# Performance work log

Hardware: AMD Instinct MI355X
Metric: run time of the kernel (lower is better)

## Reference

```python
import jax, jax.numpy as jnp
import numpy as np

N_PATCH = 15  # patch_size
M_UNITS = 16  # patches_per_batch


def setup_inputs() -> dict:
    key = jax.random.key(0)
    k1, k2, k3 = jax.random.split(key, 3)
    B, C, H, W = 64, 128, 64, 64
    x = jax.random.normal(k1, (B, C, H, W), dtype=jnp.float32)
    x_cord = jax.random.randint(k2, (B, M_UNITS), 0, W)
    y_cord = jax.random.randint(k3, (B, M_UNITS), 0, H)
    return {"x": x, "x_cord": x_cord, "y_cord": y_cord}


def reference(x, x_cord, y_cord):
    # x: [B, C, H, W]; x_cord/y_cord: [B, M] integer cell indices.
    B, C, H, W = x.shape
    n = N_PATCH
    M = x_cord.shape[1]

    lin = jnp.linspace(-1.0, 1.0, n, dtype=jnp.float32)
    gy, gx = jnp.meshgrid(lin, lin, indexing="ij")  # base_grid: gx = [..,0], gy = [..,1]

    xs = x_cord.reshape(-1).astype(jnp.float32)  # [B*M]
    ys = y_cord.reshape(-1).astype(jnp.float32)
    xs_n = (xs / (W - 1) * 2.0 - 1.0)[:, None, None]
    ys_n = (ys / (H - 1) * 2.0 - 1.0)[:, None, None]
    scale_x = (n - 1) / (W - 1)
    scale_y = (n - 1) / (H - 1)

    # NOTE: the original deliberately adds ys_norm to the x-channel and xs_norm
    # to the y-channel of the grid; we replicate that exactly.
    grid_x_ch = gx * scale_x + ys_n  # grid[..., 0] -> width coord for grid_sample
    grid_y_ch = gy * scale_y + xs_n  # grid[..., 1] -> height coord

    in_bounds = ((grid_x_ch >= -1) & (grid_x_ch <= 1)
                 & (grid_y_ch >= -1) & (grid_y_ch <= 1)).astype(x.dtype)  # [B*M, n, n]

    # grid_sample(mode='nearest', align_corners=True, padding_mode='zeros')
    ix = jnp.round((grid_x_ch + 1.0) * 0.5 * (W - 1)).astype(jnp.int32)
    iy = jnp.round((grid_y_ch + 1.0) * 0.5 * (H - 1)).astype(jnp.int32)
    valid = (ix >= 0) & (ix < W) & (iy >= 0) & (iy < H)
    ixc = jnp.clip(ix, 0, W - 1)
    iyc = jnp.clip(iy, 0, H - 1)

    b_idx = jnp.repeat(jnp.arange(B), M)[:, None, None]  # [B*M,1,1]
    # Direct gather from x (no B*M expanded copy): result [B*M, n, n, C]
    patches = x[b_idx, :, iyc, ixc]
    patches = jnp.transpose(patches, (0, 3, 1, 2))  # [B*M, C, n, n]
    patches = patches * valid[:, None, :, :].astype(x.dtype)  # zero padding

    return jnp.concatenate([patches, in_bounds[:, None, :, :]], axis=1)  # [B*M, C+1, n, n]
```

## Files before the change

### kernel.cpp

```cpp
#include <hip/hip_runtime.h>


constexpr int NP    = 15;
constexpr int NPOS  = NP * NP;
constexpr int CH    = 128;
constexpr int HH    = 64, WW = 64;
constexpr int PLANE = HH * WW;
constexpr int MPB   = 16;
constexpr unsigned PER_PATCH = (CH + 1) * NPOS;

__global__ __launch_bounds__(256)
void patch_swz(const float* __restrict__ x,
               const int* __restrict__ xcord,
               const int* __restrict__ ycord,
               float* __restrict__ out) {
  const int cg = blockIdx.x;
  const int b  = blockIdx.y;
  const int t  = threadIdx.x;

  __shared__ int    sx[MPB], sy[MPB];
  __shared__ float4 s4[HH * (WW / 4)];

  if (t < MPB) { sx[t] = xcord[b * MPB + t]; sy[t] = ycord[b * MPB + t]; }

  if (cg == CH) {
    __syncthreads();
    for (int e = t; e < MPB * NPOS; e += 256) {
      const int p   = e / NPOS;
      const int pos = e - p * NPOS;
      const int i  = pos / NP;
      const int j  = pos - i * NP;
      const int xs = sx[p], ys = sy[p];
      const int ix = ys + j - 7;
      const int iy = xs + i - 7;
      const bool v = ((unsigned)ix < (unsigned)WW) && ((unsigned)iy < (unsigned)HH);
      const bool xflip = (ix == WW - 1) && (ys < WW - 1);
      const bool yflip = (iy == HH - 1) && (xs < HH - 1);
      out[(size_t)(b * MPB + p) * PER_PATCH + (size_t)CH * NPOS + pos] =
          (v && !xflip && !yflip) ? 1.0f : 0.0f;
    }
    return;
  }

  const float4* __restrict__ src =
      reinterpret_cast<const float4*>(x + ((size_t)b * CH + cg) * PLANE);
#pragma unroll
  for (int k = t; k < PLANE / 4; k += 256) {
    const int row = k >> 4;
    const int c4  = k & 15;
    s4[(row << 4) + ((c4 + 2 * row) & 15)] = src[k];
  }
  __syncthreads();

  const float* __restrict__ s = reinterpret_cast<const float*>(s4);
  const size_t outbase = (size_t)b * MPB * PER_PATCH + (size_t)cg * NPOS;
  for (int e = t; e < MPB * NPOS; e += 256) {
    const int p   = e / NPOS;
    const int pos = e - p * NPOS;
    const int i  = pos / NP;
    const int j  = pos - i * NP;
    const int xs = sx[p], ys = sy[p];
    const int ix = ys + j - 7;
    const int iy = xs + i - 7;
    const bool v = ((unsigned)ix < (unsigned)WW) && ((unsigned)iy < (unsigned)HH);
    float val = 0.0f;
    if (v) {
      const int c4 = ix >> 2, w = ix & 3;
      val = s[(iy << 6) + (((c4 + 2 * iy) & 15) << 2) + w];
    }
    out[outbase + (size_t)p * PER_PATCH + pos] = val;
  }
}

extern "C" void kernel_launch(void* const* d_in, const int* in_sizes, int n_in,
                              void* d_out, int out_size, void* d_ws, size_t ws_size,
                              hipStream_t stream) {
  const float* x  = (const float*)d_in[0];
  const int*   xc = (const int*)d_in[1];
  const int*   yc = (const int*)d_in[2];
  float* outp = (float*)d_out;

  dim3 grid(CH + 1, 64);
  patch_swz<<<grid, 256, 0, stream>>>(x, xc, yc, outp);
}
```

Baseline: 46.91 us.

## Precompute gather offset tables and use direct global-to-LDS loads with vector stores

Adds a prepass kernel that computes per-patch LDS offsets and in-bounds masks into global tables, so the main kernel no longer does per-element index arithmetic. The plane is loaded with global_load_lds, and the swizzle is applied on the source side. Each wave writes one patch per step using 4-wide stores. This trades an extra kernel launch and table reads for less ALU work, cheaper staging and wider writes, with the risk of misaligned vector stores because 225-float patches are not 16-byte aligned.

```diff
diff --git a/kernel.cpp b/kernel.cpp
--- a/kernel.cpp
+++ b/kernel.cpp
@@ -7,37 +7,59 @@
 constexpr int HH    = 64, WW = 64;
 constexpr int PLANE = HH * WW;
 constexpr int MPB   = 16;
+constexpr int TPAD  = 228;
 constexpr unsigned PER_PATCH = (CH + 1) * NPOS;
 
+__device__ int   g_tbl[1024 * TPAD];
+__device__ float g_ibt[1024 * TPAD];
+
+typedef int   i4  __attribute__((ext_vector_type(4)));
+typedef float f4v __attribute__((ext_vector_type(4)));
+typedef float f4a __attribute__((ext_vector_type(4), aligned(4)));
+
 __global__ __launch_bounds__(256)
-void patch_swz(const float* __restrict__ x,
-               const int* __restrict__ xcord,
-               const int* __restrict__ ycord,
-               float* __restrict__ out) {
+void build_tables(const int* __restrict__ xc, const int* __restrict__ yc) {
+  const int p = blockIdx.x, t = threadIdx.x;
+  if (t >= TPAD) return;
+  int off = -1; float ib = 0.0f;
+  if (t < NPOS) {
+    const int i  = t / NP;
+    const int j  = t - i * NP;
+    const int xs = xc[p], ys = yc[p];
+    const int ix = ys + j - 7;
+    const int iy = xs + i - 7;
+    const bool v = ((unsigned)ix < (unsigned)WW) && ((unsigned)iy < (unsigned)HH);
+    if (v) {
+      const int c4 = ix >> 2, w = ix & 3;
+      off = (iy << 6) + (((c4 + iy) & 15) << 2) + w;
+    }
+    const bool xf = (ix == WW - 1) && (ys < WW - 1);
+    const bool yf = (iy == HH - 1) && (xs < HH - 1);
+    ib = (v && !xf && !yf) ? 1.0f : 0.0f;
+  }
+  g_tbl[p * TPAD + t] = off;
+  g_ibt[p * TPAD + t] = ib;
+}
+
+__global__ __launch_bounds__(256)
+void patch_tbl(const float* __restrict__ x, float* __restrict__ out) {
   const int cg = blockIdx.x;
   const int b  = blockIdx.y;
   const int t  = threadIdx.x;
+  const int wv = t >> 6, lane = t & 63;
 
-  __shared__ int    sx[MPB], sy[MPB];
-  __shared__ float4 s4[HH * (WW / 4)];
-
-  if (t < MPB) { sx[t] = xcord[b * MPB + t]; sy[t] = ycord[b * MPB + t]; }
+  __shared__ float s[PLANE];
 
   if (cg == CH) {
-    __syncthreads();
-    for (int e = t; e < MPB * NPOS; e += 256) {
-      const int p   = e / NPOS;
-      const int pos = e - p * NPOS;
-      const int i  = pos / NP;
-      const int j  = pos - i * NP;
-      const int xs = sx[p], ys = sy[p];
-      const int ix = ys + j - 7;
-      const int iy = xs + i - 7;
-      const bool v = ((unsigned)ix < (unsigned)WW) && ((unsigned)iy < (unsigned)HH);
-      const bool xflip = (ix == WW - 1) && (ys < WW - 1);
-      const bool yflip = (iy == HH - 1) && (xs < HH - 1);
-      out[(size_t)(b * MPB + p) * PER_PATCH + (size_t)CH * NPOS + pos] =
-          (v && !xflip && !yflip) ? 1.0f : 0.0f;
+    for (int m = wv; m < MPB; m += 4) {
+      const int p = b * MPB + m;
+      const size_t S = (size_t)p * PER_PATCH + (size_t)CH * NPOS;
+      if (lane < 56) {
+        const f4v o = *reinterpret_cast<const f4v*>(&g_ibt[p * TPAD + 4 * lane]);
+        *reinterpret_cast<f4a*>(out + S + 4 * (size_t)lane) = o;
+      } else if (lane == 56) {
+        out[S + 224] = g_ibt[p * TPAD + 224];
+      }
     }
     return;
   }
@@ -45,30 +67,34 @@
   const float4* __restrict__ src =
       reinterpret_cast<const float4*>(x + ((size_t)b * CH + cg) * PLANE);
 #pragma unroll
-  for (int k = t; k < PLANE / 4; k += 256) {
-    const int row = k >> 4;
-    const int c4  = k & 15;
-    s4[(row << 4) + ((c4 + 2 * row) & 15)] = src[k];
+  for (int k = 0; k < 4; ++k) {
+    const int slot  = k * 256 + t;
+    const int row   = slot >> 4;
+    const int c4p   = slot & 15;
+    const int srcf4 = (row << 4) + ((c4p - row) & 15);
+    float4* ldsbase = reinterpret_cast<float4*>(s) + k * 256 + (t & 192);
+    __builtin_amdgcn_global_load_lds(
+        (const __attribute__((address_space(1))) void*)(src + srcf4),
+        (__attribute__((address_space(3))) void*)ldsbase,
+        16, 0, 0);
   }
   __syncthreads();
 
-  const float* __restrict__ s = reinterpret_cast<const float*>(s4);
-  const size_t outbase = (size_t)b * MPB * PER_PATCH + (size_t)cg * NPOS;
-  for (int e = t; e < MPB * NPOS; e += 256) {
-    const int p   = e / NPOS;
-    const int pos = e - p * NPOS;
-    const int i  = pos / NP;
-    const int j  = pos - i * NP;
-    const int xs = sx[p], ys = sy[p];
-    const int ix = ys + j - 7;
-    const int iy = xs + i - 7;
-    const bool v = ((unsigned)ix < (unsigned)WW) && ((unsigned)iy < (unsigned)HH);
-    float val = 0.0f;
-    if (v) {
-      const int c4 = ix >> 2, w = ix & 3;
-      val = s[(iy << 6) + (((c4 + 2 * iy) & 15) << 2) + w];
+  for (int m = wv; m < MPB; m += 4) {
+    const int p = b * MPB + m;
+    const size_t S = (size_t)p * PER_PATCH + (size_t)cg * NPOS;
+    if (lane < 56) {
+      const i4 o4 = *reinterpret_cast<const i4*>(&g_tbl[p * TPAD + 4 * lane]);
+      f4v o;
+      o.x = (o4.x >= 0) ? s[o4.x & (PLANE - 1)] : 0.0f;
+      o.y = (o4.y >= 0) ? s[o4.y & (PLANE - 1)] : 0.0f;
+      o.z = (o4.z >= 0) ? s[o4.z & (PLANE - 1)] : 0.0f;
+      o.w = (o4.w >= 0) ? s[o4.w & (PLANE - 1)] : 0.0f;
+      *reinterpret_cast<f4a*>(out + S + 4 * (size_t)lane) = o;
+    } else if (lane == 56) {
+      const int off = g_tbl[p * TPAD + 224];
+      out[S + 224] = (off >= 0) ? s[off & (PLANE - 1)] : 0.0f;
     }
-    out[outbase + (size_t)p * PER_PATCH + pos] = val;
   }
 }
 
@@ -80,6 +106,7 @@
   const int*   yc = (const int*)d_in[2];
   float* outp = (float*)d_out;
 
+  build_tables<<<1024, 256, 0, stream>>>(xc, yc);
   dim3 grid(CH + 1, 64);
-  patch_swz<<<grid, 256, 0, stream>>>(x, xc, yc, outp);
+  patch_tbl<<<grid, 256, 0, stream>>>(x, outp);
 }
```

Result: slower. 53.32 us (+13.7%).
